# Optimization experiments

Measured on AMD Instinct MI355X. Metric: run time of the kernel, lower is better.

## Reference

```python
import jax, jax.numpy as jnp
import numpy as np

B = 32768
F = 256
H = 8


def setup_inputs() -> dict:
    key = jax.random.key(0)
    ks = jax.random.split(key, 6)
    input_tensor = jax.random.normal(ks[0], (B, F), dtype=jnp.float32)
    # Per-feature MLP params: Dense(1->8), Dense(8->8), Dense(8->1, no bias)
    W1 = jax.random.normal(ks[1], (F, H), dtype=jnp.float32) * 0.5   # [F, 8] (input dim 1 folded)
    b1 = jax.random.normal(ks[2], (F, H), dtype=jnp.float32) * 0.1
    W2 = jax.random.normal(ks[3], (F, H, H), dtype=jnp.float32) * (1.0 / np.sqrt(H))
    b2 = jax.random.normal(ks[4], (F, H), dtype=jnp.float32) * 0.1
    W3 = jax.random.normal(ks[5], (F, H), dtype=jnp.float32) * (1.0 / np.sqrt(H))  # [F, 8] (output dim 1 folded)
    return {"input_tensor": input_tensor, "W1": W1, "b1": b1, "W2": W2, "b2": b2, "W3": W3}


def reference(input_tensor, W1, b1, W2, b2, W3):
    # Batched over features instead of a Python loop over F tiny MLPs.
    # h1: [B, F, H] = relu(x * W1 + b1), scalar input per feature
    h1 = jax.nn.relu(input_tensor[:, :, None] * W1[None, :, :] + b1[None, :, :])
    # h2: [B, F, H]
    h2 = jax.nn.relu(jnp.einsum('bfh,fhk->bfk', h1, W2) + b2[None, :, :])
    # per-feature scalar contribution w: [B, F]
    w = jnp.einsum('bfh,fh->bf', h2, W3)
    output = jnp.sum(w, axis=1, keepdims=True)  # [B, 1]
    return (output, w)
```

## Files before the change

### kernel.cpp

```cpp
#include <hip/hip_runtime.h>

#define NB 32768
#define NF 256
#define NH 8
#define ROWS_PER_BLOCK 32

__global__ __launch_bounds__(256, 2) void NAM_49314814493074_kernel(
    const float* __restrict__ input,
    const float* __restrict__ W1,
    const float* __restrict__ b1,
    const float* __restrict__ W2,
    const float* __restrict__ b2,
    const float* __restrict__ W3,
    float* __restrict__ out_sum,
    float* __restrict__ out_w)
{
    __shared__ float sred[ROWS_PER_BLOCK][NF];

    const int f = threadIdx.x;
    const int row0 = blockIdx.x * ROWS_PER_BLOCK;

    const float* xin = input + (size_t)row0 * NF + f;
    float* wout = out_w + (size_t)row0 * NF + f;

    float xv[ROWS_PER_BLOCK];
    #pragma unroll
    for (int r = 0; r < ROWS_PER_BLOCK; ++r)
        xv[r] = xin[(size_t)r * NF];

    float w1[NH], bb1[NH], bb2[NH], w3[NH];
    float w2[NH][NH];
    {
        const float4* p1  = reinterpret_cast<const float4*>(W1 + (size_t)f * NH);
        const float4* pb1 = reinterpret_cast<const float4*>(b1 + (size_t)f * NH);
        const float4* pb2 = reinterpret_cast<const float4*>(b2 + (size_t)f * NH);
        const float4* p3  = reinterpret_cast<const float4*>(W3 + (size_t)f * NH);
        float4 a, b;
        a = p1[0]; b = p1[1];
        w1[0]=a.x; w1[1]=a.y; w1[2]=a.z; w1[3]=a.w; w1[4]=b.x; w1[5]=b.y; w1[6]=b.z; w1[7]=b.w;
        a = pb1[0]; b = pb1[1];
        bb1[0]=a.x; bb1[1]=a.y; bb1[2]=a.z; bb1[3]=a.w; bb1[4]=b.x; bb1[5]=b.y; bb1[6]=b.z; bb1[7]=b.w;
        a = pb2[0]; b = pb2[1];
        bb2[0]=a.x; bb2[1]=a.y; bb2[2]=a.z; bb2[3]=a.w; bb2[4]=b.x; bb2[5]=b.y; bb2[6]=b.z; bb2[7]=b.w;
        a = p3[0]; b = p3[1];
        w3[0]=a.x; w3[1]=a.y; w3[2]=a.z; w3[3]=a.w; w3[4]=b.x; w3[5]=b.y; w3[6]=b.z; w3[7]=b.w;

        const float4* p2 = reinterpret_cast<const float4*>(W2 + (size_t)f * NH * NH);
        #pragma unroll
        for (int h = 0; h < NH; ++h) {
            float4 c0 = p2[h * 2 + 0];
            float4 c1 = p2[h * 2 + 1];
            w2[h][0]=c0.x; w2[h][1]=c0.y; w2[h][2]=c0.z; w2[h][3]=c0.w;
            w2[h][4]=c1.x; w2[h][5]=c1.y; w2[h][6]=c1.z; w2[h][7]=c1.w;
        }
    }

    #pragma unroll
    for (int r = 0; r < ROWS_PER_BLOCK; ++r) {
        const float x = xv[r];

        float h1[NH];
        #pragma unroll
        for (int h = 0; h < NH; ++h)
            h1[h] = fmaxf(fmaf(x, w1[h], bb1[h]), 0.0f);

        float acc[NH];
        #pragma unroll
        for (int k = 0; k < NH; ++k) acc[k] = bb2[k];
        #pragma unroll
        for (int h = 0; h < NH; ++h) {
            #pragma unroll
            for (int k = 0; k < NH; ++k)
                acc[k] = fmaf(h1[h], w2[h][k], acc[k]);
        }

        float s = 0.0f;
        #pragma unroll
        for (int k = 0; k < NH; ++k)
            s = fmaf(fmaxf(acc[k], 0.0f), w3[k], s);

        wout[(size_t)r * NF] = s;
        sred[r][f] = s;
    }

    __syncthreads();

    const int wave = threadIdx.x >> 6;
    const int lane = threadIdx.x & 63;
    #pragma unroll
    for (int rr = 0; rr < ROWS_PER_BLOCK / 4; ++rr) {
        const int r = wave * (ROWS_PER_BLOCK / 4) + rr;
        const float4 q = reinterpret_cast<const float4*>(&sred[r][0])[lane];
        float v = q.x + q.y + q.z + q.w;
        #pragma unroll
        for (int off = 32; off > 0; off >>= 1)
            v += __shfl_xor(v, off, 64);
        if (lane == 0)
            out_sum[row0 + r] = v;
    }
}

extern "C" void kernel_launch(void* const* d_in, const int* in_sizes, int n_in,
                              void* d_out, int out_size, void* d_ws, size_t ws_size,
                              hipStream_t stream) {
    const float* input = (const float*)d_in[0];
    const float* W1    = (const float*)d_in[1];
    const float* b1    = (const float*)d_in[2];
    const float* W2    = (const float*)d_in[3];
    const float* b2    = (const float*)d_in[4];
    const float* W3    = (const float*)d_in[5];

    float* out = (float*)d_out;
    float* out_sum = out;
    float* out_w   = out + NB;

    dim3 grid(NB / ROWS_PER_BLOCK);
    dim3 block(NF);
    NAM_49314814493074_kernel<<<grid, block, 0, stream>>>(
        input, W1, b1, W2, b2, W3, out_sum, out_w);
}
```

Baseline: 106.3 us.

## Split each feature's hidden units across two threads with shuffle combine

Each feature is now handled by a pair of threads, each computing four of the eight second-layer outputs, and the partial sums are combined with a lane shuffle. The block grows to 512 threads and the final row-sum reduction is spread across eight waves. This lowers per-thread register use and serial FMA chains to raise occupancy and latency hiding. In exchange it adds shuffle work, duplicates the first-layer computation in both threads of a pair, and makes the loads and stores less coalesced, since both threads of a pair read the same input element and only one of them writes.

```diff
diff --git a/kernel.cpp b/kernel.cpp
--- a/kernel.cpp
+++ b/kernel.cpp
@@ -4,8 +4,9 @@
 #define NF 256
 #define NH 8
 #define ROWS_PER_BLOCK 32
+#define NTHREADS 512
 
-__global__ __launch_bounds__(256, 2) void NAM_49314814493074_kernel(
+__global__ __launch_bounds__(NTHREADS, 4) void NAM_49314814493074_kernel(
     const float* __restrict__ input,
     const float* __restrict__ W1,
     const float* __restrict__ b1,
@@ -17,7 +18,9 @@
 {
     __shared__ float sred[ROWS_PER_BLOCK][NF];
 
-    const int f = threadIdx.x;
+    const int t    = threadIdx.x;
+    const int f    = t >> 1;
+    const int half = t & 1;
     const int row0 = blockIdx.x * ROWS_PER_BLOCK;
 
     const float* xin = input + (size_t)row0 * NF + f;
@@ -28,30 +31,27 @@
     for (int r = 0; r < ROWS_PER_BLOCK; ++r)
         xv[r] = xin[(size_t)r * NF];
 
-    float w1[NH], bb1[NH], bb2[NH], w3[NH];
-    float w2[NH][NH];
+    float w1[NH], bb1[NH];
+    float w2[NH][4], bb2[4], w3[4];
     {
         const float4* p1  = reinterpret_cast<const float4*>(W1 + (size_t)f * NH);
         const float4* pb1 = reinterpret_cast<const float4*>(b1 + (size_t)f * NH);
-        const float4* pb2 = reinterpret_cast<const float4*>(b2 + (size_t)f * NH);
-        const float4* p3  = reinterpret_cast<const float4*>(W3 + (size_t)f * NH);
         float4 a, b;
         a = p1[0]; b = p1[1];
         w1[0]=a.x; w1[1]=a.y; w1[2]=a.z; w1[3]=a.w; w1[4]=b.x; w1[5]=b.y; w1[6]=b.z; w1[7]=b.w;
         a = pb1[0]; b = pb1[1];
         bb1[0]=a.x; bb1[1]=a.y; bb1[2]=a.z; bb1[3]=a.w; bb1[4]=b.x; bb1[5]=b.y; bb1[6]=b.z; bb1[7]=b.w;
-        a = pb2[0]; b = pb2[1];
-        bb2[0]=a.x; bb2[1]=a.y; bb2[2]=a.z; bb2[3]=a.w; bb2[4]=b.x; bb2[5]=b.y; bb2[6]=b.z; bb2[7]=b.w;
-        a = p3[0]; b = p3[1];
-        w3[0]=a.x; w3[1]=a.y; w3[2]=a.z; w3[3]=a.w; w3[4]=b.x; w3[5]=b.y; w3[6]=b.z; w3[7]=b.w;
+
+        float4 c = reinterpret_cast<const float4*>(b2 + (size_t)f * NH)[half];
+        bb2[0]=c.x; bb2[1]=c.y; bb2[2]=c.z; bb2[3]=c.w;
+        c = reinterpret_cast<const float4*>(W3 + (size_t)f * NH)[half];
+        w3[0]=c.x; w3[1]=c.y; w3[2]=c.z; w3[3]=c.w;
 
         const float4* p2 = reinterpret_cast<const float4*>(W2 + (size_t)f * NH * NH);
         #pragma unroll
         for (int h = 0; h < NH; ++h) {
-            float4 c0 = p2[h * 2 + 0];
-            float4 c1 = p2[h * 2 + 1];
-            w2[h][0]=c0.x; w2[h][1]=c0.y; w2[h][2]=c0.z; w2[h][3]=c0.w;
-            w2[h][4]=c1.x; w2[h][5]=c1.y; w2[h][6]=c1.z; w2[h][7]=c1.w;
+            float4 d = p2[h * 2 + half];
+            w2[h][0]=d.x; w2[h][1]=d.y; w2[h][2]=d.z; w2[h][3]=d.w;
         }
     }
 
@@ -64,32 +64,35 @@
         for (int h = 0; h < NH; ++h)
             h1[h] = fmaxf(fmaf(x, w1[h], bb1[h]), 0.0f);
 
-        float acc[NH];
+        float acc[4];
         #pragma unroll
-        for (int k = 0; k < NH; ++k) acc[k] = bb2[k];
+        for (int k = 0; k < 4; ++k) acc[k] = bb2[k];
         #pragma unroll
         for (int h = 0; h < NH; ++h) {
             #pragma unroll
-            for (int k = 0; k < NH; ++k)
+            for (int k = 0; k < 4; ++k)
                 acc[k] = fmaf(h1[h], w2[h][k], acc[k]);
         }
 
         float s = 0.0f;
         #pragma unroll
-        for (int k = 0; k < NH; ++k)
+        for (int k = 0; k < 4; ++k)
             s = fmaf(fmaxf(acc[k], 0.0f), w3[k], s);
+        s += __shfl_xor(s, 1, 64);
 
-        wout[(size_t)r * NF] = s;
-        sred[r][f] = s;
+        if (half == 0)
+            wout[(size_t)r * NF] = s;
+        else
+            sred[r][f] = s;
     }
 
     __syncthreads();
 
-    const int wave = threadIdx.x >> 6;
-    const int lane = threadIdx.x & 63;
+    const int wave = t >> 6;
+    const int lane = t & 63;
     #pragma unroll
-    for (int rr = 0; rr < ROWS_PER_BLOCK / 4; ++rr) {
-        const int r = wave * (ROWS_PER_BLOCK / 4) + rr;
+    for (int rr = 0; rr < ROWS_PER_BLOCK / 8; ++rr) {
+        const int r = wave * (ROWS_PER_BLOCK / 8) + rr;
         const float4 q = reinterpret_cast<const float4*>(&sred[r][0])[lane];
         float v = q.x + q.y + q.z + q.w;
         #pragma unroll
@@ -115,7 +118,7 @@
     float* out_w   = out + NB;
 
     dim3 grid(NB / ROWS_PER_BLOCK);
-    dim3 block(NF);
+    dim3 block(NTHREADS);
     NAM_49314814493074_kernel<<<grid, block, 0, stream>>>(
         input, W1, b1, W2, b2, W3, out_sum, out_w);
 }
```

New measurement: 110.0 us. +3.5%, slower.

## Use packed f32x2 FMA math and write w outputs as float4 from shared memory

Applied to the files above, without the earlier changes.

Processes two rows at once with 2-wide float vectors so the compiler can emit packed FMA/max instructions (v_pk_fma_f32) that halve the VALU instruction count. It loads the inputs after the weights, in two halves. The per-thread scalar stores of w are dropped; w is instead written as float4 from the shared reduction buffer during the reduction phase. Register pressure may rise, and packed ops need splat operands, which could add moves.

```diff
diff --git a/kernel.cpp b/kernel.cpp
--- a/kernel.cpp
+++ b/kernel.cpp
@@ -4,6 +4,14 @@
 #define NF 256
 #define NH 8
 #define ROWS_PER_BLOCK 32
+#define NPAIR (ROWS_PER_BLOCK / 2)
+
+
+typedef float f32x2 __attribute__((ext_vector_type(2)));
+
+static __device__ __forceinline__ f32x2 splat2(float v) {
+    f32x2 r; r.x = v; r.y = v; return r;
+}
 
 __global__ __launch_bounds__(256, 2) void NAM_49314814493074_kernel(
     const float* __restrict__ input,
@@ -19,14 +27,6 @@
 
     const int f = threadIdx.x;
     const int row0 = blockIdx.x * ROWS_PER_BLOCK;
-
-    const float* xin = input + (size_t)row0 * NF + f;
-    float* wout = out_w + (size_t)row0 * NF + f;
-
-    float xv[ROWS_PER_BLOCK];
-    #pragma unroll
-    for (int r = 0; r < ROWS_PER_BLOCK; ++r)
-        xv[r] = xin[(size_t)r * NF];
 
     float w1[NH], bb1[NH], bb2[NH], w3[NH];
     float w2[NH][NH];
@@ -55,33 +55,58 @@
         }
     }
 
+    const float* xin = input + (size_t)row0 * NF + f;
+
+    f32x2 xA[NPAIR / 2], xB[NPAIR / 2];
     #pragma unroll
-    for (int r = 0; r < ROWS_PER_BLOCK; ++r) {
-        const float x = xv[r];
+    for (int p = 0; p < NPAIR / 2; ++p) {
+        xA[p].x = xin[(size_t)(2 * p) * NF];
+        xA[p].y = xin[(size_t)(2 * p + 1) * NF];
+    }
+    #pragma unroll
+    for (int p = 0; p < NPAIR / 2; ++p) {
+        xB[p].x = xin[(size_t)(16 + 2 * p) * NF];
+        xB[p].y = xin[(size_t)(16 + 2 * p + 1) * NF];
+    }
 
-        float h1[NH];
+    const f32x2 zero2 = splat2(0.0f);
+
+    auto computePairs = [&](f32x2 (&xb)[NPAIR / 2], int pair0) {
         #pragma unroll
-        for (int h = 0; h < NH; ++h)
-            h1[h] = fmaxf(fmaf(x, w1[h], bb1[h]), 0.0f);
+        for (int p = 0; p < NPAIR / 2; ++p) {
+            const f32x2 x = xb[p];
 
-        float acc[NH];
-        #pragma unroll
-        for (int k = 0; k < NH; ++k) acc[k] = bb2[k];
-        #pragma unroll
-        for (int h = 0; h < NH; ++h) {
+            f32x2 h1[NH];
+            #pragma unroll
+            for (int h = 0; h < NH; ++h)
+                h1[h] = __builtin_elementwise_max(
+                    __builtin_elementwise_fma(x, splat2(w1[h]), splat2(bb1[h])), zero2);
+
+            f32x2 acc[NH];
             #pragma unroll
             for (int k = 0; k < NH; ++k)
-                acc[k] = fmaf(h1[h], w2[h][k], acc[k]);
+                acc[k] = __builtin_elementwise_fma(h1[0], splat2(w2[0][k]), splat2(bb2[k]));
+            #pragma unroll
+            for (int h = 1; h < NH; ++h) {
+                #pragma unroll
+                for (int k = 0; k < NH; ++k)
+                    acc[k] = __builtin_elementwise_fma(h1[h], splat2(w2[h][k]), acc[k]);
+            }
+
+            f32x2 s = zero2;
+            #pragma unroll
+            for (int k = 0; k < NH; ++k)
+                s = __builtin_elementwise_fma(
+                    __builtin_elementwise_max(acc[k], zero2), splat2(w3[k]), s);
+
+            const int r = (pair0 + p) * 2;
+            sred[r][f]     = s.x;
+            sred[r + 1][f] = s.y;
         }
+    };
 
-        float s = 0.0f;
-        #pragma unroll
-        for (int k = 0; k < NH; ++k)
-            s = fmaf(fmaxf(acc[k], 0.0f), w3[k], s);
-
-        wout[(size_t)r * NF] = s;
-        sred[r][f] = s;
-    }
+    computePairs(xA, 0);
+    computePairs(xB, NPAIR / 2);
 
     __syncthreads();
 
@@ -91,6 +116,7 @@
     for (int rr = 0; rr < ROWS_PER_BLOCK / 4; ++rr) {
         const int r = wave * (ROWS_PER_BLOCK / 4) + rr;
         const float4 q = reinterpret_cast<const float4*>(&sred[r][0])[lane];
+        reinterpret_cast<float4*>(out_w + (size_t)(row0 + r) * NF)[lane] = q;
         float v = q.x + q.y + q.z + q.w;
         #pragma unroll
         for (int off = 32; off > 0; off >>= 1)
```

Result: no change. 105.8 us (-0.5%).
